# Kernel tuning notes

Measured on AMD Instinct MI355X. Metric: run time of the kernel, lower is better.

The kernel has to match this reference:

```python
import jax, jax.numpy as jnp
import numpy as np

B, T, D = 1, 4096, 1024
H, DK, DV, L = 16, 64, 64, 32
ROT_SCALE = 1.0  # rotary_pos_scale default


def _rotate_half(x):
    # '... (j d) -> ... j d' with j=2, then cat((-x2, x1))
    x1, x2 = jnp.split(x, 2, axis=-1)
    return jnp.concatenate((-x2, x1), axis=-1)


def _apply_rope(freqs, x, scale):
    # freqs: [T, L] broadcasts over leading dims of x [..., T, L]
    return x * jnp.cos(freqs) * scale + _rotate_half(x) * jnp.sin(freqs) * scale


def setup_inputs() -> dict:
    key = jax.random.key(0)
    ks = jax.random.split(key, 9)
    q = jax.random.normal(ks[0], (B, T, D), jnp.float32)
    k = jax.random.normal(ks[1], (B, T, D), jnp.float32)
    v = jax.random.normal(ks[2], (B, T, D), jnp.float32)
    mask = jnp.tril(jnp.ones((T, T), dtype=bool))  # causal [T, T]
    rotary_freqs = jax.random.normal(ks[3], (T, L), jnp.float32)
    s = 0.02
    w_q = jax.random.normal(ks[4], (H * DK, D), jnp.float32) * s
    w_k = jax.random.normal(ks[5], (H * DK, D), jnp.float32) * s
    w_v = jax.random.normal(ks[6], (H * DV, D), jnp.float32) * s
    w_o = jax.random.normal(ks[7], (D, H * DV), jnp.float32) * s
    return {"q": q, "k": k, "v": v, "mask": mask, "rotary_freqs": rotary_freqs,
            "w_q": w_q, "w_k": w_k, "w_v": w_v, "w_o": w_o}


def reference(q, k, v, mask, rotary_freqs, w_q, w_k, w_v, w_o):
    # project and split heads: '... T (H k) -> ... H T k'
    def heads(x, w, dh):
        y = jnp.einsum('btd,ed->bte', x, w)
        return y.reshape(B, T, H, dh).transpose(0, 2, 1, 3)  # [B,H,T,dh]

    q_i = heads(q, w_q, DK)
    k_i = heads(k, w_k, DK)
    v_i = heads(v, w_v, DV)

    # rotary pos emb on first L dims of q, k AND v (unusual: v too)
    q_scale, k_scale = ROT_SCALE, ROT_SCALE ** (-1.0)

    def rope(x, scale):
        xl, xr = x[..., :L], x[..., L:]
        return jnp.concatenate((_apply_rope(rotary_freqs, xl, scale), xr), axis=-1)

    q_i = rope(q_i, q_scale)
    k_i = rope(k_i, k_scale)
    v_i = rope(v_i, k_scale)

    s_qk = jnp.einsum('bhik,bhjk->bhij', q_i, k_i) / (DK ** 0.5)
    neg = -jnp.finfo(s_qk.dtype).max
    s_qk = jnp.where(mask, s_qk, neg)  # mask broadcasts [T,T] -> [B,H,T,T]
    attn = jax.nn.softmax(s_qk, axis=-1)
    vals = jnp.einsum('bhij,bhjv->bhiv', attn, v_i)
    vals = vals.transpose(0, 2, 1, 3).reshape(B, T, H * DV)  # '... H T v -> ... T (H v)'
    out = jnp.einsum('bte,oe->bto', vals, w_o)
    return out
```

## Files before the change

### kernel.cpp

```cpp
#include <hip/hip_runtime.h>

typedef unsigned short u16;
typedef unsigned int u32;
typedef short bf16x8 __attribute__((ext_vector_type(8)));
typedef float f32x4 __attribute__((ext_vector_type(4)));
typedef unsigned short u16x4 __attribute__((ext_vector_type(4)));
typedef unsigned short u16x8 __attribute__((ext_vector_type(8)));

__device__ __forceinline__ u16 f32_to_bf16(float f) {
    u32 u = __float_as_uint(f);
    u += 0x7FFFu + ((u >> 16) & 1u);
    return (u16)(u >> 16);
}
__device__ __forceinline__ short f32_to_bf16_trunc(float f) {
    return (short)(__float_as_uint(f) >> 16);
}

#if __has_builtin(__builtin_amdgcn_exp2f)
#define EXP2(x) __builtin_amdgcn_exp2f(x)
#else
#define EXP2(x) __expf((x) * 0.69314718056f)
#endif

__device__ __forceinline__ void gl_lds16(const u16* g, u16* l) {
    __builtin_amdgcn_global_load_lds(
        (const __attribute__((address_space(1))) u32*)g,
        (__attribute__((address_space(3))) u32*)l, 16, 0, 0);
}


struct CastArgs {
    const float* src[8];
    u16* dst[8];
    int n4[8];
};

__global__ __launch_bounds__(256) void cast_kernel(CastArgs a) {
    const int y = blockIdx.y;
    const int n4 = a.n4[y];
    if (y == 7) {
        const float* s = a.src[7];
        float* c  = (float*)a.dst[7];
        float* sn = c + 131072;
        for (int i = blockIdx.x * blockDim.x + threadIdx.x; i < n4; i += gridDim.x * blockDim.x) {
            f32x4 v = *(const f32x4*)&s[(size_t)i * 4];
            f32x4 cv, sv;
            #pragma unroll
            for (int j = 0; j < 4; j++) {
                float ss, cc;
                __sincosf(v[j], &ss, &cc);
                sv[j] = ss; cv[j] = cc;
            }
            *(f32x4*)&c[(size_t)i * 4]  = cv;
            *(f32x4*)&sn[(size_t)i * 4] = sv;
        }
        return;
    }
    const float* s = a.src[y];
    u16* d = a.dst[y];
    for (int i = blockIdx.x * blockDim.x + threadIdx.x; i < n4; i += gridDim.x * blockDim.x) {
        f32x4 v = *(const f32x4*)&s[(size_t)i * 4];
        u16x4 o = { f32_to_bf16(v[0]), f32_to_bf16(v[1]), f32_to_bf16(v[2]), f32_to_bf16(v[3]) };
        *(u16x4*)&d[(size_t)i * 4] = o;
    }
}

#define GK 1024
#define GN 1024
#define GM 4096

__global__ __launch_bounds__(256) void gemm_rope(
    const u16* __restrict__ A0, const u16* __restrict__ A1, const u16* __restrict__ A2,
    const u16* __restrict__ W0, const u16* __restrict__ W1, const u16* __restrict__ W2,
    u16* __restrict__ C0, u16* __restrict__ C1, u16* __restrict__ C2,
    const float* __restrict__ freqs, const float* __restrict__ csT)
{
    __shared__ u16 SM[16384];

    const int z = blockIdx.z;
    const u16* A = (z == 0) ? A0 : ((z == 1) ? A1 : A2);
    const u16* W = (z == 0) ? W0 : ((z == 1) ? W1 : W2);
    u16* Cb      = (z == 0) ? C0 : ((z == 1) ? C1 : C2);
    const float ascale = (z == 0) ? 0.18033688f : 1.0f;

    const int tid  = threadIdx.x;
    const int w    = tid >> 6;
    const int lane = tid & 63;
    const int quad = lane >> 4;
    const int l16  = lane & 15;
    const int m0 = blockIdx.x * 128;
    const int n0 = blockIdx.y * 128;
    const int wm = (w >> 1) * 64;
    const int wn = (w & 1) * 64;

    const int sr = tid >> 2;
    const int sc = (((tid & 3) ^ ((tid >> 3) & 3))) * 8;
    const size_t aoff0 = (size_t)(m0 + sr) * GK + sc;
    const size_t aoff1 = aoff0 + (size_t)64 * GK;
    const size_t boff0 = (size_t)(n0 + sr) * GK + sc;
    const size_t boff1 = boff0 + (size_t)64 * GK;

    const int csw = (quad ^ ((l16 >> 1) & 3)) * 8;

    f32x4 acc[4][4];
    for (int i = 0; i < 4; i++)
        for (int j = 0; j < 4; j++) acc[i][j] = 0.f;

    {
        u16* Ab = SM;
        gl_lds16(A + aoff0, &Ab[w * 512]);
        gl_lds16(A + aoff1, &Ab[2048 + w * 512]);
        gl_lds16(W + boff0, &Ab[4096 + w * 512]);
        gl_lds16(W + boff1, &Ab[4096 + 2048 + w * 512]);
    }

    for (int it = 0; it < 32; ++it) {
        __syncthreads();
        if (it < 31) {
            const int k0 = (it + 1) * 32;
            u16* Ab = SM + ((it + 1) & 1) * 8192;
            gl_lds16(A + aoff0 + k0, &Ab[w * 512]);
            gl_lds16(A + aoff1 + k0, &Ab[2048 + w * 512]);
            gl_lds16(W + boff0 + k0, &Ab[4096 + w * 512]);
            gl_lds16(W + boff1 + k0, &Ab[4096 + 2048 + w * 512]);
        }
        const u16* As = SM + (it & 1) * 8192;
        const u16* Bs = As + 4096;

        bf16x8 af[4], bfr[4];
        for (int t = 0; t < 4; t++) {
            af[t]  = *(const bf16x8*)&As[(wm + t * 16 + l16) * 32 + csw];
            bfr[t] = *(const bf16x8*)&Bs[(wn + t * 16 + l16) * 32 + csw];
        }
        for (int mt = 0; mt < 4; mt++)
            for (int nt = 0; nt < 4; nt++)
                acc[mt][nt] = __builtin_amdgcn_mfma_f32_16x16x32_bf16(
                    af[mt], bfr[nt], acc[mt][nt], 0, 0, 0);
    }
    __syncthreads();
    u16* tr = SM + w * 1152;

    const int hh = (n0 + wn) >> 6;
    const size_t tb = (size_t)hh * 262144 + (size_t)((m0 + wm) >> 6) * 4096;
    const float* snT = csT ? (csT + 131072) : (const float*)0;

    if (z != 2) {
        for (int mt = 0; mt < 4; mt++) {
            #pragma unroll
            for (int r = 0; r < 4; r++) {
                int m = m0 + wm + mt * 16 + quad * 4 + r;
                float v0 = acc[mt][0][r];
                float v1 = acc[mt][1][r];
                float s0, c0, s1, c1;
                if (csT) {
                    c0 = csT[m * 32 + l16];      s0 = snT[m * 32 + l16];
                    c1 = csT[m * 32 + 16 + l16]; s1 = snT[m * 32 + 16 + l16];
                } else {
                    __sincosf(freqs[m * 32 + l16], &s0, &c0);
                    __sincosf(freqs[m * 32 + 16 + l16], &s1, &c1);
                }
                int row = quad * 4 + r;
                tr[row * 72 + l16]      = f32_to_bf16((v0 * c0 - v1 * s0) * ascale);
                tr[row * 72 + 16 + l16] = f32_to_bf16((v1 * c1 + v0 * s1) * ascale);
                tr[row * 72 + 32 + l16] = f32_to_bf16(acc[mt][2][r] * ascale);
                tr[row * 72 + 48 + l16] = f32_to_bf16(acc[mt][3][r] * ascale);
            }
            u16x8 va = *(const u16x8*)&tr[l16 * 72 + quad * 16];
            u16x8 vb = *(const u16x8*)&tr[l16 * 72 + quad * 16 + 8];
            if (z == 0) {
                size_t base = (size_t)(m0 + wm + mt * 16 + l16) * GN + n0 + wn + quad * 16;
                *(u16x8*)&Cb[base]     = va;
                *(u16x8*)&Cb[base + 8] = vb;
            } else {
                size_t base = tb + (size_t)(quad >> 1) * 2048
                            + (size_t)(mt * 16 + l16) * 32 + (quad & 1) * 16;
                *(u16x8*)&Cb[base]     = va;
                *(u16x8*)&Cb[base + 8] = vb;
            }
        }
    } else {
        for (int mt = 0; mt < 4; mt++) {
            float o0[4], o1[4];
            for (int r = 0; r < 4; r++) {
                int m = m0 + wm + mt * 16 + quad * 4 + r;
                float v0 = acc[mt][0][r];
                float v1 = acc[mt][1][r];
                float s0, c0, s1, c1;
                if (csT) {
                    c0 = csT[m * 32 + l16];      s0 = snT[m * 32 + l16];
                    c1 = csT[m * 32 + 16 + l16]; s1 = snT[m * 32 + 16 + l16];
                } else {
                    __sincosf(freqs[m * 32 + l16], &s0, &c0);
                    __sincosf(freqs[m * 32 + 16 + l16], &s1, &c1);
                }
                o0[r] = v0 * c0 - v1 * s0;
                o1[r] = v1 * c1 + v0 * s1;
            }
            const int ks = mt >> 1;
            const int sl = 4 * (mt & 1) + 8 * quad;
            const size_t hb = tb + (size_t)ks * 2048 + sl;
            u16x4 u;
            u = { f32_to_bf16(o0[0]), f32_to_bf16(o0[1]), f32_to_bf16(o0[2]), f32_to_bf16(o0[3]) };
            *(u16x4*)&Cb[hb + (size_t)l16 * 32] = u;
            u = { f32_to_bf16(o1[0]), f32_to_bf16(o1[1]), f32_to_bf16(o1[2]), f32_to_bf16(o1[3]) };
            *(u16x4*)&Cb[hb + (size_t)(16 + l16) * 32] = u;
            u = { f32_to_bf16(acc[mt][2][0]), f32_to_bf16(acc[mt][2][1]),
                  f32_to_bf16(acc[mt][2][2]), f32_to_bf16(acc[mt][2][3]) };
            *(u16x4*)&Cb[hb + (size_t)(32 + l16) * 32] = u;
            u = { f32_to_bf16(acc[mt][3][0]), f32_to_bf16(acc[mt][3][1]),
                  f32_to_bf16(acc[mt][3][2]), f32_to_bf16(acc[mt][3][3]) };
            *(u16x4*)&Cb[hb + (size_t)(48 + l16) * 32] = u;
        }
    }
}

__global__ __launch_bounds__(256) void gemm_out(
    const u16* __restrict__ A, const u16* __restrict__ W, float* __restrict__ C)
{
    __shared__ u16 SM[12288];

    const int tid  = threadIdx.x;
    const int w    = tid >> 6;
    const int lane = tid & 63;
    const int quad = lane >> 4;
    const int l16  = lane & 15;
    const int m0 = blockIdx.x * 64;
    const int n0 = blockIdx.y * 128;
    const int wm = (w >> 1) * 32;
    const int wn = (w & 1) * 64;

    const int sr = tid >> 2;
    const int sc = (((tid & 3) ^ ((tid >> 3) & 3))) * 8;
    const size_t aoff  = (size_t)(m0 + sr) * GK + sc;
    const size_t boff0 = (size_t)(n0 + sr) * GK + sc;
    const size_t boff1 = boff0 + (size_t)64 * GK;

    const int csw = (quad ^ ((l16 >> 1) & 3)) * 8;

    f32x4 acc[2][4];
    for (int i = 0; i < 2; i++)
        for (int j = 0; j < 4; j++) acc[i][j] = 0.f;

    {
        u16* Ab = SM;
        gl_lds16(A + aoff,  &Ab[w * 512]);
        gl_lds16(W + boff0, &Ab[2048 + w * 512]);
        gl_lds16(W + boff1, &Ab[2048 + 2048 + w * 512]);
    }

    for (int it = 0; it < 32; ++it) {
        __syncthreads();
        if (it < 31) {
            const int k0 = (it + 1) * 32;
            u16* Ab = SM + ((it + 1) & 1) * 6144;
            gl_lds16(A + aoff + k0,  &Ab[w * 512]);
            gl_lds16(W + boff0 + k0, &Ab[2048 + w * 512]);
            gl_lds16(W + boff1 + k0, &Ab[2048 + 2048 + w * 512]);
        }
        const u16* As = SM + (it & 1) * 6144;
        const u16* Bs = As + 2048;

        bf16x8 af[2], bfr[4];
        for (int t = 0; t < 2; t++)
            af[t] = *(const bf16x8*)&As[(wm + t * 16 + l16) * 32 + csw];
        for (int t = 0; t < 4; t++)
            bfr[t] = *(const bf16x8*)&Bs[(wn + t * 16 + l16) * 32 + csw];
        for (int mt = 0; mt < 2; mt++)
            for (int nt = 0; nt < 4; nt++)
                acc[mt][nt] = __builtin_amdgcn_mfma_f32_16x16x32_bf16(
                    af[mt], bfr[nt], acc[mt][nt], 0, 0, 0);
    }
    __syncthreads();

    float* tr = (float*)SM + w * 1088;
    for (int mt = 0; mt < 2; mt++) {
        #pragma unroll
        for (int nt = 0; nt < 4; nt++)
            #pragma unroll
            for (int r = 0; r < 4; r++)
                tr[(quad * 4 + r) * 68 + nt * 16 + l16] = acc[mt][nt][r];
        size_t base = (size_t)(m0 + wm + mt * 16 + l16) * GN + n0 + wn + quad * 16;
        #pragma unroll
        for (int c = 0; c < 4; c++) {
            f32x4 v = *(const f32x4*)&tr[l16 * 68 + quad * 16 + c * 4];
            *(f32x4*)&C[base + c * 4] = v;
        }
    }
}

__global__ __launch_bounds__(256, 3) void attn_kernel(
    const u16* __restrict__ Qb, const u16* __restrict__ KT,
    const u16* __restrict__ VTg, u16* __restrict__ valsb)
{
    __shared__ __align__(16) u16 KV[2][8192];
    __shared__ __align__(16) float EX[4352];

    const int tid  = threadIdx.x;
    const int w    = tid >> 6;
    const int lane = tid & 63;
    const int quad = lane >> 4;
    const int l16  = lane & 15;
    const int HD = 1024;

    const int id = blockIdx.x;
    const int h  = (id & 7) * 2 + ((id >> 3) & 1);
    const int qb = 63 - (id >> 4);

    const u16* kt = KT  + (size_t)h * 262144;
    const u16* vt = VTg + (size_t)h * 262144;

    const int wq = w >> 1;
    const int wk = w & 1;

    const int dmaoff = (lane >> 2) * 32 + ((lane & 3) ^ ((lane >> 3) & 3)) * 8;
    const int csw = (quad ^ ((l16 >> 1) & 3)) * 8;

    bf16x8 ones;
    #pragma unroll
    for (int i = 0; i < 8; i++) ones[i] = (short)0x3F80;
    const f32x4 seed = { -23.0831204f, -23.0831204f, -23.0831204f, -23.0831204f };

    bf16x8 bq[2][2];
    #pragma unroll
    for (int qt = 0; qt < 2; qt++) {
        const size_t qrow = (size_t)(qb * 64 + wq * 32 + qt * 16 + l16);
        bq[qt][0] = *(const bf16x8*)&Qb[qrow * HD + h * 64 + quad * 8];
        bq[qt][1] = *(const bf16x8*)&Qb[qrow * HD + h * 64 + 32 + quad * 8];
    }

    f32x4 o[2][4];
    #pragma unroll
    for (int i = 0; i < 2; i++)
        #pragma unroll
        for (int j = 0; j < 4; j++) o[i][j] = 0.f;
    f32x4 ls_acc[2];
    ls_acc[0] = 0.f;
    ls_acc[1] = 0.f;

    #pragma unroll
    for (int i = 0; i < 2; i++) {
        gl_lds16(kt + i * 2048 + w * 512 + dmaoff, &KV[0][i * 2048 + w * 512]);
        gl_lds16(vt + i * 2048 + w * 512 + dmaoff, &KV[0][4096 + i * 2048 + w * 512]);
    }

    for (int kb = 0; kb <= qb; kb++) {
        __syncthreads();
        if (kb < qb) {
            const int nb = (kb + 1) & 1;
            const u16* ksrc = kt + (size_t)(kb + 1) * 4096;
            const u16* vsrc = vt + (size_t)(kb + 1) * 4096;
            #pragma unroll
            for (int i = 0; i < 2; i++) {
                gl_lds16(ksrc + i * 2048 + w * 512 + dmaoff, &KV[nb][i * 2048 + w * 512]);
                gl_lds16(vsrc + i * 2048 + w * 512 + dmaoff, &KV[nb][4096 + i * 2048 + w * 512]);
            }
        }
        const u16* Ksb = &KV[kb & 1][0];
        const u16* Vsb = &KV[kb & 1][4096];

        bf16x8 ak[2][2];
        #pragma unroll
        for (int kt2 = 0; kt2 < 2; kt2++) {
            const int krow = wk * 32 + kt2 * 16 + l16;
            ak[kt2][0] = *(const bf16x8*)&Ksb[krow * 32 + csw];
            ak[kt2][1] = *(const bf16x8*)&Ksb[2048 + krow * 32 + csw];
        }

        f32x4 s[2][2];
        #pragma unroll
        for (int qt = 0; qt < 2; qt++)
            #pragma unroll
            for (int kt2 = 0; kt2 < 2; kt2++) {
                f32x4 z4 = seed;
                z4 = __builtin_amdgcn_mfma_f32_16x16x32_bf16(ak[kt2][0], bq[qt][0], z4, 0, 0, 0);
                s[qt][kt2] = __builtin_amdgcn_mfma_f32_16x16x32_bf16(ak[kt2][1], bq[qt][1], z4, 0, 0, 0);
            }

        if (kb == qb) {
            #pragma unroll
            for (int qt = 0; qt < 2; qt++)
                #pragma unroll
                for (int kt2 = 0; kt2 < 2; kt2++)
                    #pragma unroll
                    for (int r = 0; r < 4; r++)
                        if (wk * 32 + kt2 * 16 + quad * 4 + r > wq * 32 + qt * 16 + l16)
                            s[qt][kt2][r] = -1e30f;
        }

        bf16x8 av[4];
        #pragma unroll
        for (int nv = 0; nv < 4; nv++)
            av[nv] = *(const bf16x8*)&Vsb[wk * 2048 + (nv * 16 + l16) * 32 + csw];

        #pragma unroll
        for (int qt = 0; qt < 2; qt++)
            #pragma unroll
            for (int kt2 = 0; kt2 < 2; kt2++)
                #pragma unroll
                for (int r = 0; r < 4; r++)
                    s[qt][kt2][r] = EXP2(s[qt][kt2][r]);

        bf16x8 bp[2];
        #pragma unroll
        for (int qt = 0; qt < 2; qt++) {
            bf16x8 b = { f32_to_bf16_trunc(s[qt][0][0]), f32_to_bf16_trunc(s[qt][0][1]),
                         f32_to_bf16_trunc(s[qt][0][2]), f32_to_bf16_trunc(s[qt][0][3]),
                         f32_to_bf16_trunc(s[qt][1][0]), f32_to_bf16_trunc(s[qt][1][1]),
                         f32_to_bf16_trunc(s[qt][1][2]), f32_to_bf16_trunc(s[qt][1][3]) };
            bp[qt] = b;
        }

        #pragma unroll
        for (int qt = 0; qt < 2; qt++)
            ls_acc[qt] = __builtin_amdgcn_mfma_f32_16x16x32_bf16(
                ones, bp[qt], ls_acc[qt], 0, 0, 0);

        #pragma unroll
        for (int nv = 0; nv < 4; nv++)
            #pragma unroll
            for (int qt = 0; qt < 2; qt++)
                o[qt][nv] = __builtin_amdgcn_mfma_f32_16x16x32_bf16(
                    av[nv], bp[qt], o[qt][nv], 0, 0, 0);
    }

    const float lsum0 = ls_acc[0][0];
    const float lsum1 = ls_acc[1][0];

    float* my = EX + (w * 64 + lane) * 17;
    if (wk == 0) {
        #pragma unroll
        for (int nv = 0; nv < 4; nv++) *(f32x4*)&my[nv * 4] = o[1][nv];
        my[16] = lsum1;
    } else {
        #pragma unroll
        for (int nv = 0; nv < 4; nv++) *(f32x4*)&my[nv * 4] = o[0][nv];
        my[16] = lsum0;
    }
    __syncthreads();
    const float* pr = EX + ((w ^ 1) * 64 + lane) * 17;
    f32x4 fin[4];
    float denom;
    if (wk == 0) {
        #pragma unroll
        for (int nv = 0; nv < 4; nv++) fin[nv] = o[0][nv] + *(const f32x4*)&pr[nv * 4];
        denom = lsum0 + pr[16];
    } else {
        #pragma unroll
        for (int nv = 0; nv < 4; nv++) fin[nv] = o[1][nv] + *(const f32x4*)&pr[nv * 4];
        denom = lsum1 + pr[16];
    }
    const float inv = 1.f / denom;
    __syncthreads();

    float* myOw = EX + w * 1088;
    #pragma unroll
    for (int nv = 0; nv < 4; nv++)
        #pragma unroll
        for (int r = 0; r < 4; r++)
            myOw[l16 * 68 + nv * 16 + quad * 4 + r] = fin[nv][r] * inv;
    #pragma unroll
    for (int i = 0; i < 4; i++) {
        int row = i * 4 + quad;
        f32x4 vv = *(const f32x4*)&myOw[row * 68 + l16 * 4];
        u16x4 u = { f32_to_bf16(vv[0]), f32_to_bf16(vv[1]), f32_to_bf16(vv[2]), f32_to_bf16(vv[3]) };
        *(u16x4*)&valsb[(size_t)(qb * 64 + wq * 32 + wk * 16 + row) * HD + h * 64 + l16 * 4] = u;
    }
}

extern "C" void kernel_launch(void* const* d_in, const int* in_sizes, int n_in,
                              void* d_out, int out_size, void* d_ws, size_t ws_size,
                              hipStream_t stream) {
    const float* q     = (const float*)d_in[0];
    const float* k     = (const float*)d_in[1];
    const float* v     = (const float*)d_in[2];
    const float* freqs = (const float*)d_in[4];
    const float* wq    = (const float*)d_in[5];
    const float* wk    = (const float*)d_in[6];
    const float* wv    = (const float*)d_in[7];
    const float* wo    = (const float*)d_in[8];

    u16* B = (u16*)d_ws;
    u16* qc  = B;
    u16* kc  = B + (size_t)4194304;
    u16* vc  = B + (size_t)8388608;
    u16* wqc = B + (size_t)12582912;
    u16* wkc = B + (size_t)13631488;
    u16* wvc = B + (size_t)14680064;
    u16* woc = B + (size_t)15728640;
    u16* Qb  = B + (size_t)16777216;
    u16* KT  = B + (size_t)20971520;
    u16* VT  = B + (size_t)25165824;
    u16* valsb = qc;

    const size_t tab_off_u16 = 29360128;
    const size_t need_bytes  = 58720256 + 2 * 131072 * sizeof(float);
    float* csT = (ws_size >= need_bytes) ? (float*)(B + tab_off_u16) : (float*)0;

    CastArgs ca;
    ca.src[0] = q;  ca.dst[0] = qc;  ca.n4[0] = 1048576;
    ca.src[1] = k;  ca.dst[1] = kc;  ca.n4[1] = 1048576;
    ca.src[2] = v;  ca.dst[2] = vc;  ca.n4[2] = 1048576;
    ca.src[3] = wq; ca.dst[3] = wqc; ca.n4[3] = 262144;
    ca.src[4] = wk; ca.dst[4] = wkc; ca.n4[4] = 262144;
    ca.src[5] = wv; ca.dst[5] = wvc; ca.n4[5] = 262144;
    ca.src[6] = wo; ca.dst[6] = woc; ca.n4[6] = 262144;
    ca.src[7] = freqs; ca.dst[7] = (u16*)csT; ca.n4[7] = csT ? 32768 : 0;
    cast_kernel<<<dim3(1024, 8), 256, 0, stream>>>(ca);

    gemm_rope<<<dim3(32, 8, 3), 256, 0, stream>>>(
        qc, kc, vc, wqc, wkc, wvc, Qb, KT, VT, freqs, csT);

    attn_kernel<<<dim3(1024), 256, 0, stream>>>(Qb, KT, VT, valsb);

    gemm_out<<<dim3(64, 8), 256, 0, stream>>>(valsb, woc, (float*)d_out);
}
```

Before: 260.5 us.

## Split attention work across eight waves with 16 query rows per wave

The attention block grows from 256 to 512 threads. Each wave now handles 16 query rows and half of the key tile instead of 32 query rows, which halves per-wave MFMA and register work and doubles the number of waves per block. K/V staging is split so four waves load K and four load V. This adds more waves to hide latency, at the cost of more LDS for the reduction buffer and fewer resident blocks per CU (launch bounds go from 3 to 2).

New measurement: 258.7 us. About the same (-0.7%).

```diff
diff --git a/kernel.cpp b/kernel.cpp
--- a/kernel.cpp
+++ b/kernel.cpp
@@ -288,12 +288,12 @@
     }
 }
 
-__global__ __launch_bounds__(256, 3) void attn_kernel(
+__global__ __launch_bounds__(512, 2) void attn_kernel(
     const u16* __restrict__ Qb, const u16* __restrict__ KT,
     const u16* __restrict__ VTg, u16* __restrict__ valsb)
 {
     __shared__ __align__(16) u16 KV[2][8192];
-    __shared__ __align__(16) float EX[4352];
+    __shared__ __align__(16) float EX[8704];
 
     const int tid  = threadIdx.x;
     const int w    = tid >> 6;
@@ -311,49 +311,39 @@
 
     const int wq = w >> 1;
     const int wk = w & 1;
+    const int wr = w & 3;
 
     const int dmaoff = (lane >> 2) * 32 + ((lane & 3) ^ ((lane >> 3) & 3)) * 8;
     const int csw = (quad ^ ((l16 >> 1) & 3)) * 8;
 
+    const u16* stsrc = (w < 4) ? kt : vt;
+    const int  stdst = (w < 4) ? 0 : 4096;
+
     bf16x8 ones;
     #pragma unroll
     for (int i = 0; i < 8; i++) ones[i] = (short)0x3F80;
     const f32x4 seed = { -23.0831204f, -23.0831204f, -23.0831204f, -23.0831204f };
 
-    bf16x8 bq[2][2];
-    #pragma unroll
-    for (int qt = 0; qt < 2; qt++) {
-        const size_t qrow = (size_t)(qb * 64 + wq * 32 + qt * 16 + l16);
-        bq[qt][0] = *(const bf16x8*)&Qb[qrow * HD + h * 64 + quad * 8];
-        bq[qt][1] = *(const bf16x8*)&Qb[qrow * HD + h * 64 + 32 + quad * 8];
-    }
-
-    f32x4 o[2][4];
-    #pragma unroll
-    for (int i = 0; i < 2; i++)
-        #pragma unroll
-        for (int j = 0; j < 4; j++) o[i][j] = 0.f;
-    f32x4 ls_acc[2];
-    ls_acc[0] = 0.f;
-    ls_acc[1] = 0.f;
-
-    #pragma unroll
-    for (int i = 0; i < 2; i++) {
-        gl_lds16(kt + i * 2048 + w * 512 + dmaoff, &KV[0][i * 2048 + w * 512]);
-        gl_lds16(vt + i * 2048 + w * 512 + dmaoff, &KV[0][4096 + i * 2048 + w * 512]);
-    }
+    const size_t qrow = (size_t)(qb * 64 + wq * 16 + l16);
+    const bf16x8 bq0 = *(const bf16x8*)&Qb[qrow * HD + h * 64 + quad * 8];
+    const bf16x8 bq1 = *(const bf16x8*)&Qb[qrow * HD + h * 64 + 32 + quad * 8];
+    const int q_local = wq * 16 + l16;
+
+    f32x4 o[4];
+    #pragma unroll
+    for (int i = 0; i < 4; i++) o[i] = 0.f;
+    f32x4 ls_acc = 0.f;
+
+    gl_lds16(stsrc + wr * 512 + dmaoff,        &KV[0][stdst + wr * 512]);
+    gl_lds16(stsrc + 2048 + wr * 512 + dmaoff, &KV[0][stdst + 2048 + wr * 512]);
 
     for (int kb = 0; kb <= qb; kb++) {
         __syncthreads();
         if (kb < qb) {
             const int nb = (kb + 1) & 1;
-            const u16* ksrc = kt + (size_t)(kb + 1) * 4096;
-            const u16* vsrc = vt + (size_t)(kb + 1) * 4096;
-            #pragma unroll
-            for (int i = 0; i < 2; i++) {
-                gl_lds16(ksrc + i * 2048 + w * 512 + dmaoff, &KV[nb][i * 2048 + w * 512]);
-                gl_lds16(vsrc + i * 2048 + w * 512 + dmaoff, &KV[nb][4096 + i * 2048 + w * 512]);
-            }
+            const u16* src = stsrc + (size_t)(kb + 1) * 4096;
+            gl_lds16(src + wr * 512 + dmaoff,        &KV[nb][stdst + wr * 512]);
+            gl_lds16(src + 2048 + wr * 512 + dmaoff, &KV[nb][stdst + 2048 + wr * 512]);
         }
         const u16* Ksb = &KV[kb & 1][0];
         const u16* Vsb = &KV[kb & 1][4096];
@@ -366,90 +356,57 @@
             ak[kt2][1] = *(const bf16x8*)&Ksb[2048 + krow * 32 + csw];
         }
 
-        f32x4 s[2][2];
-        #pragma unroll
-        for (int qt = 0; qt < 2; qt++)
-            #pragma unroll
-            for (int kt2 = 0; kt2 < 2; kt2++) {
-                f32x4 z4 = seed;
-                z4 = __builtin_amdgcn_mfma_f32_16x16x32_bf16(ak[kt2][0], bq[qt][0], z4, 0, 0, 0);
-                s[qt][kt2] = __builtin_amdgcn_mfma_f32_16x16x32_bf16(ak[kt2][1], bq[qt][1], z4, 0, 0, 0);
-            }
+        f32x4 s[2];
+        #pragma unroll
+        for (int kt2 = 0; kt2 < 2; kt2++) {
+            f32x4 z4 = seed;
+            z4 = __builtin_amdgcn_mfma_f32_16x16x32_bf16(ak[kt2][0], bq0, z4, 0, 0, 0);
+            s[kt2] = __builtin_amdgcn_mfma_f32_16x16x32_bf16(ak[kt2][1], bq1, z4, 0, 0, 0);
+        }
 
         if (kb == qb) {
-            #pragma unroll
-            for (int qt = 0; qt < 2; qt++)
-                #pragma unroll
-                for (int kt2 = 0; kt2 < 2; kt2++)
-                    #pragma unroll
-                    for (int r = 0; r < 4; r++)
-                        if (wk * 32 + kt2 * 16 + quad * 4 + r > wq * 32 + qt * 16 + l16)
-                            s[qt][kt2][r] = -1e30f;
-        }
-
-        bf16x8 av[4];
-        #pragma unroll
-        for (int nv = 0; nv < 4; nv++)
-            av[nv] = *(const bf16x8*)&Vsb[wk * 2048 + (nv * 16 + l16) * 32 + csw];
-
-        #pragma unroll
-        for (int qt = 0; qt < 2; qt++)
             #pragma unroll
             for (int kt2 = 0; kt2 < 2; kt2++)
                 #pragma unroll
                 for (int r = 0; r < 4; r++)
-                    s[qt][kt2][r] = EXP2(s[qt][kt2][r]);
-
-        bf16x8 bp[2];
-        #pragma unroll
-        for (int qt = 0; qt < 2; qt++) {
-            bf16x8 b = { f32_to_bf16_trunc(s[qt][0][0]), f32_to_bf16_trunc(s[qt][0][1]),
-                         f32_to_bf16_trunc(s[qt][0][2]), f32_to_bf16_trunc(s[qt][0][3]),
-                         f32_to_bf16_trunc(s[qt][1][0]), f32_to_bf16_trunc(s[qt][1][1]),
-                         f32_to_bf16_trunc(s[qt][1][2]), f32_to_bf16_trunc(s[qt][1][3]) };
-            bp[qt] = b;
-        }
-
-        #pragma unroll
-        for (int qt = 0; qt < 2; qt++)
-            ls_acc[qt] = __builtin_amdgcn_mfma_f32_16x16x32_bf16(
-                ones, bp[qt], ls_acc[qt], 0, 0, 0);
-
+                    if (wk * 32 + kt2 * 16 + quad * 4 + r > q_local) s[kt2][r] = -1e30f;
+        }
+
+        bf16x8 av[4];
         #pragma unroll
         for (int nv = 0; nv < 4; nv++)
+            av[nv] = *(const bf16x8*)&Vsb[wk * 2048 + (nv * 16 + l16) * 32 + csw];
+
+        #pragma unroll
+        for (int kt2 = 0; kt2 < 2; kt2++)
             #pragma unroll
-            for (int qt = 0; qt < 2; qt++)
-                o[qt][nv] = __builtin_amdgcn_mfma_f32_16x16x32_bf16(
-                    av[nv], bp[qt], o[qt][nv], 0, 0, 0);
-    }
-
-    const float lsum0 = ls_acc[0][0];
-    const float lsum1 = ls_acc[1][0];
+            for (int r = 0; r < 4; r++)
+                s[kt2][r] = EXP2(s[kt2][r]);
+
+        bf16x8 bp = { f32_to_bf16_trunc(s[0][0]), f32_to_bf16_trunc(s[0][1]),
+                      f32_to_bf16_trunc(s[0][2]), f32_to_bf16_trunc(s[0][3]),
+                      f32_to_bf16_trunc(s[1][0]), f32_to_bf16_trunc(s[1][1]),
+                      f32_to_bf16_trunc(s[1][2]), f32_to_bf16_trunc(s[1][3]) };
+
+        ls_acc = __builtin_amdgcn_mfma_f32_16x16x32_bf16(ones, bp, ls_acc, 0, 0, 0);
+
+        #pragma unroll
+        for (int nv = 0; nv < 4; nv++)
+            o[nv] = __builtin_amdgcn_mfma_f32_16x16x32_bf16(av[nv], bp, o[nv], 0, 0, 0);
+    }
+
+    const float lsum = ls_acc[0];
 
     float* my = EX + (w * 64 + lane) * 17;
-    if (wk == 0) {
-        #pragma unroll
-        for (int nv = 0; nv < 4; nv++) *(f32x4*)&my[nv * 4] = o[1][nv];
-        my[16] = lsum1;
-    } else {
-        #pragma unroll
-        for (int nv = 0; nv < 4; nv++) *(f32x4*)&my[nv * 4] = o[0][nv];
-        my[16] = lsum0;
-    }
+    #pragma unroll
+    for (int nv = 0; nv < 4; nv++) *(f32x4*)&my[nv * 4] = o[nv];
+    my[16] = lsum;
     __syncthreads();
     const float* pr = EX + ((w ^ 1) * 64 + lane) * 17;
     f32x4 fin[4];
-    float denom;
-    if (wk == 0) {
-        #pragma unroll
-        for (int nv = 0; nv < 4; nv++) fin[nv] = o[0][nv] + *(const f32x4*)&pr[nv * 4];
-        denom = lsum0 + pr[16];
-    } else {
-        #pragma unroll
-        for (int nv = 0; nv < 4; nv++) fin[nv] = o[1][nv] + *(const f32x4*)&pr[nv * 4];
-        denom = lsum1 + pr[16];
-    }
-    const float inv = 1.f / denom;
+    #pragma unroll
+    for (int nv = 0; nv < 4; nv++) fin[nv] = o[nv] + *(const f32x4*)&pr[nv * 4];
+    const float inv = 1.f / (lsum + pr[16]);
     __syncthreads();
 
     float* myOw = EX + w * 1088;
@@ -459,11 +416,11 @@
         for (int r = 0; r < 4; r++)
             myOw[l16 * 68 + nv * 16 + quad * 4 + r] = fin[nv][r] * inv;
     #pragma unroll
-    for (int i = 0; i < 4; i++) {
-        int row = i * 4 + quad;
+    for (int i = 0; i < 2; i++) {
+        int row = (wk * 2 + i) * 4 + quad;
         f32x4 vv = *(const f32x4*)&myOw[row * 68 + l16 * 4];
         u16x4 u = { f32_to_bf16(vv[0]), f32_to_bf16(vv[1]), f32_to_bf16(vv[2]), f32_to_bf16(vv[3]) };
-        *(u16x4*)&valsb[(size_t)(qb * 64 + wq * 32 + wk * 16 + row) * HD + h * 64 + l16 * 4] = u;
+        *(u16x4*)&valsb[(size_t)(qb * 64 + wq * 16 + row) * HD + h * 64 + l16 * 4] = u;
     }
 }
 
@@ -510,7 +467,7 @@
     gemm_rope<<<dim3(32, 8, 3), 256, 0, stream>>>(
         qc, kc, vc, wqc, wkc, wvc, Qb, KT, VT, freqs, csT);
 
-    attn_kernel<<<dim3(1024), 256, 0, stream>>>(Qb, KT, VT, valsb);
+    attn_kernel<<<dim3(1024), 512, 0, stream>>>(Qb, KT, VT, valsb);
 
     gemm_out<<<dim3(64, 8), 256, 0, stream>>>(valsb, woc, (float*)d_out);
 }
```
